# Kernel tuning notes

Measured on AMD Instinct MI355X. Metric: run time of the kernel, lower is better.

## Reference

```python
import jax, jax.numpy as jnp
import numpy as np

EPS = 1e-12  # F.normalize default eps


def _heatmap_pool(part_features, blocks):
    # part_features: [B, N, C]
    B, N, C = part_features.shape
    heatmap = jnp.mean(part_features, axis=-1)              # [B, N]
    arg = jnp.argsort(-heatmap, axis=1)                     # descending order
    x_sort = jnp.take_along_axis(part_features, arg[:, :, None], axis=1)  # [B, N, C]
    split_each = int(N / blocks)
    split_list = [split_each] * (blocks - 1)
    split_list.append(N - sum(split_list))
    offs = np.concatenate([[0], np.cumsum(split_list)])
    means = [jnp.mean(x_sort[:, offs[i]:offs[i + 1], :], axis=1) for i in range(blocks)]
    return jnp.stack(means, axis=2)                         # [B, C, blocks]


def _l2norm(x):
    n = jnp.sqrt(jnp.sum(x * x, axis=-1, keepdims=True))
    return x / jnp.maximum(n, EPS)


def setup_inputs() -> dict:
    key = jax.random.key(0)
    k1, k2 = jax.random.split(key)
    B, C, H, W = 64, 768, 24, 24
    return {
        "image_features1": jax.random.normal(k1, (B, C, H, W), dtype=jnp.float32),
        "image_features2": jax.random.normal(k2, (B, C, H, W), dtype=jnp.float32),
        "logit_scale": jnp.ones((1,), dtype=jnp.float32),
        "weights": jnp.ones((1,), dtype=jnp.float32),
        "blocks": 3,
    }


def reference(image_features1, image_features2, logit_scale, weights, blocks):
    B, C = image_features1.shape[0], image_features1.shape[1]
    f1 = image_features1.reshape(B, C, -1).transpose(0, 2, 1)  # [B, N, C]
    f2 = image_features2.reshape(B, C, -1).transpose(0, 2, 1)
    h1 = _heatmap_pool(f1, blocks)                             # [B, C, blocks]
    h2 = _heatmap_pool(f2, blocks)
    # cat blocks along channel dim: [B, C*blocks]
    b1 = jnp.concatenate([h1[:, :, i] for i in range(blocks)], axis=-1)
    b2 = jnp.concatenate([h2[:, :, i] for i in range(blocks)], axis=-1)
    n1 = _l2norm(b1)
    n2 = _l2norm(b2)
    return jnp.mean((n1 - n2) ** 2)
```

## Files before the change

### kernel.cpp

```cpp
#include <hip/hip_runtime.h>

#define NB 64
#define NC 768
#define NN 576
#define NF4 144

#define HR 16
#define HCH 48
#define GR 16
#define GCH 48

#define OFF_HM   0ull
#define SZ_HM    (2ull*NB*HCH*NN*8ull)
#define OFF_GID  (OFF_HM + SZ_HM)
#define SZ_GID   (2ull*NB*NN)
#define OFF_GP   (OFF_GID + SZ_GID)
#define SZ_GP    (2ull*NB*NC*12ull*4ull)
#define OFF_PB   (OFF_GP + SZ_GP)

__global__ __launch_bounds__(192, 8) void k_heat(const float* __restrict__ f1,
                                                 const float* __restrict__ f2,
                                                 double* __restrict__ hm) {
    int bx    = blockIdx.x;
    int inpb  = bx / HCH;
    int chunk = bx - inpb * HCH;
    int b     = inpb & (NB - 1);
    int inp   = inpb >> 6;
    const float* f = (inp ? f2 : f1) + (size_t)b * NC * NN + (size_t)chunk * HR * NN;
    int t = threadIdx.x;
    double d0 = 0, d1 = 0, d2 = 0;
    #pragma unroll
    for (int r0 = 0; r0 < HR; r0 += 8) {
        float v[24];
        #pragma unroll
        for (int rr = 0; rr < 8; ++rr) {
            const float* row = f + (size_t)(r0 + rr) * NN + t;
            v[rr * 3 + 0] = row[0];
            v[rr * 3 + 1] = row[192];
            v[rr * 3 + 2] = row[384];
        }
        #pragma unroll
        for (int rr = 0; rr < 8; ++rr) {
            d0 += (double)v[rr * 3 + 0];
            d1 += (double)v[rr * 3 + 1];
            d2 += (double)v[rr * 3 + 2];
        }
    }
    double* o = hm + (size_t)bx * NN;
    o[t] = d0; o[t + 192] = d1; o[t + 384] = d2;
}

__global__ __launch_bounds__(576) void k_rank(const double* __restrict__ hm,
                                              unsigned char* __restrict__ gid8) {
    int bx = blockIdx.x;
    int t  = threadIdx.x;
    const double* p = hm + (size_t)bx * HCH * NN + t;
    double h = 0;
    #pragma unroll
    for (int c0 = 0; c0 < HCH; c0 += 16) {
        double v[16];
        #pragma unroll
        for (int ch = 0; ch < 16; ++ch) v[ch] = p[(size_t)(c0 + ch) * NN];
        #pragma unroll
        for (int ch = 0; ch < 16; ++ch) h += v[ch];
    }
    __shared__ double hs[NN];
    hs[t] = h;
    __syncthreads();
    int cnt = 0;
    for (int j = 0; j < NN; ++j) {
        double hj = hs[j];
        cnt += (hj > h) ? 1 : ((hj == h && j < t) ? 1 : 0);
    }
    gid8[(size_t)bx * NN + t] = (cnt >= 384) ? 2 : ((cnt >= 192) ? 1 : 0);
}

__global__ __launch_bounds__(256, 8) void k_gsum(const float* __restrict__ f1,
                                                 const float* __restrict__ f2,
                                                 const unsigned* __restrict__ gidw,
                                                 float* __restrict__ gp) {
    int bx    = blockIdx.x;
    int inpb  = bx / GCH;
    int chunk = bx - inpb * GCH;
    int b     = inpb & (NB - 1);
    int inp   = inpb >> 6;
    const float4* plane = (const float4*)((inp ? f2 : f1) + (size_t)b * NC * NN);
    int t = threadIdx.x;
    int w = t >> 6, l = t & 63;
    int sub = l & 15, rr = l >> 4;

    unsigned g[9];
    const unsigned* gw = gidw + (size_t)inpb * NF4;
    #pragma unroll
    for (int k = 0; k < 9; ++k) g[k] = gw[sub + 16 * k];

    int c = chunk * GR + w * 4 + rr;
    const float4* row = plane + (size_t)c * NF4 + sub;
    float4 v[9];
    #pragma unroll
    for (int k = 0; k < 9; ++k) v[k] = row[16 * k];
    float sa = 0.f, s1 = 0.f, s2 = 0.f;
    #pragma unroll
    for (int k = 0; k < 9; ++k) {
        unsigned gwk = g[k];
        float x; unsigned gg;
        x = v[k].x; gg = gwk & 0xffu;         sa += x; s1 += (gg >= 1u) ? x : 0.f; s2 += (gg == 2u) ? x : 0.f;
        x = v[k].y; gg = (gwk >> 8) & 0xffu;  sa += x; s1 += (gg >= 1u) ? x : 0.f; s2 += (gg == 2u) ? x : 0.f;
        x = v[k].z; gg = (gwk >> 16) & 0xffu; sa += x; s1 += (gg >= 1u) ? x : 0.f; s2 += (gg == 2u) ? x : 0.f;
        x = v[k].w; gg = gwk >> 24;           sa += x; s1 += (gg >= 1u) ? x : 0.f; s2 += (gg == 2u) ? x : 0.f;
    }
    sa += __shfl_xor(sa, 4); s1 += __shfl_xor(s1, 4); s2 += __shfl_xor(s2, 4);
    sa += __shfl_xor(sa, 8); s1 += __shfl_xor(s1, 8); s2 += __shfl_xor(s2, 8);
    if (sub < 4) {
        float* o = gp + (size_t)inpb * NC * 12 + (size_t)c * 12;
        o[0 * 4 + sub] = sa - s1;
        o[1 * 4 + sub] = s1 - s2;
        o[2 * 4 + sub] = s2;
    }
}

__global__ __launch_bounds__(256) void k_mse(const float* __restrict__ gp,
                                             double* __restrict__ pb) {
    int b = blockIdx.x;
    int t = threadIdx.x;
    int w = t >> 6, l = t & 63;
    const float4* s1 = (const float4*)(gp + (size_t)b * NC * 12);
    const float4* s2 = (const float4*)(gp + (size_t)(NB + b) * NC * 12);

    double v1[9], v2[9];
    double q1 = 0, q2 = 0;
    #pragma unroll
    for (int k = 0; k < 9; ++k) {
        int e = t + 256 * k;
        float4 a = s1[e], c4 = s2[e];
        v1[k] = ((double)a.x + (double)a.y + (double)a.z + (double)a.w) * (1.0 / 192.0);
        v2[k] = ((double)c4.x + (double)c4.y + (double)c4.z + (double)c4.w) * (1.0 / 192.0);
        q1 += v1[k] * v1[k];
        q2 += v2[k] * v2[k];
    }
    #pragma unroll
    for (int m = 32; m; m >>= 1) { q1 += __shfl_xor(q1, m); q2 += __shfl_xor(q2, m); }
    __shared__ double red1[4], red2[4];
    if (l == 0) { red1[w] = q1; red2[w] = q2; }
    __syncthreads();
    q1 = red1[0] + red1[1] + red1[2] + red1[3];
    q2 = red2[0] + red2[1] + red2[2] + red2[3];
    double inv1 = 1.0 / fmax(sqrt(q1), 1e-12);
    double inv2 = 1.0 / fmax(sqrt(q2), 1e-12);

    double acc = 0;
    #pragma unroll
    for (int k = 0; k < 9; ++k) {
        double d = v1[k] * inv1 - v2[k] * inv2;
        acc += d * d;
    }
    #pragma unroll
    for (int m = 32; m; m >>= 1) acc += __shfl_xor(acc, m);
    __syncthreads();
    if (l == 0) red1[w] = acc;
    __syncthreads();
    if (t == 0) pb[b] = red1[0] + red1[1] + red1[2] + red1[3];
}

__global__ __launch_bounds__(64) void k_final(const double* __restrict__ pb,
                                              float* __restrict__ out) {
    int l = threadIdx.x;
    double v = pb[l];
    #pragma unroll
    for (int m = 32; m; m >>= 1) v += __shfl_xor(v, m);
    if (l == 0) out[0] = (float)(v / ((double)NB * 3.0 * (double)NC));
}

extern "C" void kernel_launch(void* const* d_in, const int* in_sizes, int n_in,
                              void* d_out, int out_size, void* d_ws, size_t ws_size,
                              hipStream_t stream) {
    (void)in_sizes; (void)n_in; (void)out_size; (void)ws_size;
    const float* f1 = (const float*)d_in[0];
    const float* f2 = (const float*)d_in[1];
    float* out = (float*)d_out;
    char* ws = (char*)d_ws;

    double*        hm   = (double*)(ws + OFF_HM);
    unsigned char* gid8 = (unsigned char*)(ws + OFF_GID);
    float*         gp   = (float*)(ws + OFF_GP);
    double*        pb   = (double*)(ws + OFF_PB);

    k_heat <<<2 * NB * HCH, 192, 0, stream>>>(f1, f2, hm);
    k_rank <<<2 * NB,       576, 0, stream>>>(hm, gid8);
    k_gsum <<<2 * NB * GCH, 256, 0, stream>>>(f1, f2, (const unsigned*)gid8, gp);
    k_mse  <<<NB,           256, 0, stream>>>(gp, pb);
    k_final<<<1,            64,  0, stream>>>(pb, out);
}
```

Baseline: 307.8 us.

## Pipeline heatmap and group-sum passes across the two inputs in a mixed kernel

Handles the two feature tensors in a staggered order. The heatmap pass for input 1 runs in the same launch as the group-sum pass for input 2, with blocks interleaved 3:4, so their memory traffic overlaps and the small serial rank kernel is hidden between larger launches. Group-sum blocks shrink to 192 threads covering 12 channels each (64 chunks per image), and launch bounds drop to 4 blocks per CU for the mixed kernels. The cost is one extra rank launch and more launches overall.

```diff
diff --git a/kernel.cpp b/kernel.cpp
--- a/kernel.cpp
+++ b/kernel.cpp
@@ -7,8 +7,8 @@
 
 #define HR 16
 #define HCH 48
-#define GR 16
-#define GCH 48
+#define GR 12
+#define GCH 64
 
 #define OFF_HM   0ull
 #define SZ_HM    (2ull*NB*HCH*NN*8ull)
@@ -18,23 +18,17 @@
 #define SZ_GP    (2ull*NB*NC*12ull*4ull)
 #define OFF_PB   (OFF_GP + SZ_GP)
 
-__global__ __launch_bounds__(192, 8) void k_heat(const float* __restrict__ f1,
-                                                 const float* __restrict__ f2,
-                                                 double* __restrict__ hm) {
-    int bx    = blockIdx.x;
-    int inpb  = bx / HCH;
-    int chunk = bx - inpb * HCH;
-    int b     = inpb & (NB - 1);
-    int inp   = inpb >> 6;
-    const float* f = (inp ? f2 : f1) + (size_t)b * NC * NN + (size_t)chunk * HR * NN;
-    int t = threadIdx.x;
+__device__ __forceinline__ void heat_body(const float* __restrict__ f,
+                                          double* __restrict__ hm,
+                                          int b, int chunk, int t) {
+    const float* p = f + (size_t)b * NC * NN + (size_t)chunk * HR * NN;
     double d0 = 0, d1 = 0, d2 = 0;
     #pragma unroll
     for (int r0 = 0; r0 < HR; r0 += 8) {
         float v[24];
         #pragma unroll
         for (int rr = 0; rr < 8; ++rr) {
-            const float* row = f + (size_t)(r0 + rr) * NN + t;
+            const float* row = p + (size_t)(r0 + rr) * NN + t;
             v[rr * 3 + 0] = row[0];
             v[rr * 3 + 1] = row[192];
             v[rr * 3 + 2] = row[384];
@@ -46,53 +40,22 @@
             d2 += (double)v[rr * 3 + 2];
         }
     }
-    double* o = hm + (size_t)bx * NN;
+    double* o = hm + ((size_t)b * HCH + chunk) * NN;
     o[t] = d0; o[t + 192] = d1; o[t + 384] = d2;
 }
 
-__global__ __launch_bounds__(576) void k_rank(const double* __restrict__ hm,
-                                              unsigned char* __restrict__ gid8) {
-    int bx = blockIdx.x;
-    int t  = threadIdx.x;
-    const double* p = hm + (size_t)bx * HCH * NN + t;
-    double h = 0;
-    #pragma unroll
-    for (int c0 = 0; c0 < HCH; c0 += 16) {
-        double v[16];
-        #pragma unroll
-        for (int ch = 0; ch < 16; ++ch) v[ch] = p[(size_t)(c0 + ch) * NN];
-        #pragma unroll
-        for (int ch = 0; ch < 16; ++ch) h += v[ch];
-    }
-    __shared__ double hs[NN];
-    hs[t] = h;
-    __syncthreads();
-    int cnt = 0;
-    for (int j = 0; j < NN; ++j) {
-        double hj = hs[j];
-        cnt += (hj > h) ? 1 : ((hj == h && j < t) ? 1 : 0);
-    }
-    gid8[(size_t)bx * NN + t] = (cnt >= 384) ? 2 : ((cnt >= 192) ? 1 : 0);
-}
-
-__global__ __launch_bounds__(256, 8) void k_gsum(const float* __restrict__ f1,
-                                                 const float* __restrict__ f2,
-                                                 const unsigned* __restrict__ gidw,
-                                                 float* __restrict__ gp) {
-    int bx    = blockIdx.x;
-    int inpb  = bx / GCH;
-    int chunk = bx - inpb * GCH;
-    int b     = inpb & (NB - 1);
-    int inp   = inpb >> 6;
-    const float4* plane = (const float4*)((inp ? f2 : f1) + (size_t)b * NC * NN);
-    int t = threadIdx.x;
+__device__ __forceinline__ void gsum_body(const float* __restrict__ f,
+                                          const unsigned* __restrict__ gw,
+                                          float* __restrict__ gp,
+                                          int b, int chunk, int t) {
+    const float4* plane = (const float4*)(f + (size_t)b * NC * NN);
     int w = t >> 6, l = t & 63;
     int sub = l & 15, rr = l >> 4;
 
     unsigned g[9];
-    const unsigned* gw = gidw + (size_t)inpb * NF4;
-    #pragma unroll
-    for (int k = 0; k < 9; ++k) g[k] = gw[sub + 16 * k];
+    const unsigned* gwb = gw + (size_t)b * NF4;
+    #pragma unroll
+    for (int k = 0; k < 9; ++k) g[k] = gwb[sub + 16 * k];
 
     int c = chunk * GR + w * 4 + rr;
     const float4* row = plane + (size_t)c * NF4 + sub;
@@ -112,11 +75,66 @@
     sa += __shfl_xor(sa, 4); s1 += __shfl_xor(s1, 4); s2 += __shfl_xor(s2, 4);
     sa += __shfl_xor(sa, 8); s1 += __shfl_xor(s1, 8); s2 += __shfl_xor(s2, 8);
     if (sub < 4) {
-        float* o = gp + (size_t)inpb * NC * 12 + (size_t)c * 12;
+        float* o = gp + (size_t)b * NC * 12 + (size_t)c * 12;
         o[0 * 4 + sub] = sa - s1;
         o[1 * 4 + sub] = s1 - s2;
         o[2 * 4 + sub] = s2;
     }
+}
+
+__global__ __launch_bounds__(192, 8) void k_heat(const float* __restrict__ f,
+                                                 double* __restrict__ hm) {
+    int bx = blockIdx.x;
+    int b = bx / HCH, chunk = bx - b * HCH;
+    heat_body(f, hm, b, chunk, threadIdx.x);
+}
+
+__global__ __launch_bounds__(192, 4) void k_mix(const float* __restrict__ fB,
+                                                double* __restrict__ hmB,
+                                                const float* __restrict__ fA,
+                                                const unsigned* __restrict__ gwA,
+                                                float* __restrict__ gpA) {
+    int bx = blockIdx.x, t = threadIdx.x;
+    int grp = bx / 7, r = bx - grp * 7;
+    if (r < 4) {
+        int gb = grp * 4 + r;
+        gsum_body(fA, gwA, gpA, gb >> 6, gb & 63, t);
+    } else {
+        int hb = grp * 3 + (r - 4);
+        heat_body(fB, hmB, hb / HCH, hb % HCH, t);
+    }
+}
+
+__global__ __launch_bounds__(192, 4) void k_gsum(const float* __restrict__ f,
+                                                 const unsigned* __restrict__ gw,
+                                                 float* __restrict__ gp) {
+    int bx = blockIdx.x;
+    gsum_body(f, gw, gp, bx >> 6, bx & 63, threadIdx.x);
+}
+
+__global__ __launch_bounds__(576) void k_rank(const double* __restrict__ hm,
+                                              unsigned char* __restrict__ gid8) {
+    int b = blockIdx.x;
+    int t = threadIdx.x;
+    const double* p = hm + (size_t)b * HCH * NN + t;
+    double h = 0;
+    #pragma unroll
+    for (int c0 = 0; c0 < HCH; c0 += 16) {
+        double v[16];
+        #pragma unroll
+        for (int ch = 0; ch < 16; ++ch) v[ch] = p[(size_t)(c0 + ch) * NN];
+        #pragma unroll
+        for (int ch = 0; ch < 16; ++ch) h += v[ch];
+    }
+    __shared__ double hs[NN];
+    hs[t] = h;
+    __syncthreads();
+    int cnt = 0;
+    for (int j = 0; j < NN; ++j) {
+        double hj = hs[j];
+        cnt += (hj > h) ? 1 : ((hj == h && j < t) ? 1 : 0);
+    }
+    gid8[(size_t)b * NN + t] = (cnt >= 384) ? 2 : ((cnt >= 192) ? 1 : 0);
 }
 
 __global__ __launch_bounds__(256) void k_mse(const float* __restrict__ gp,
@@ -180,14 +198,19 @@
     float* out = (float*)d_out;
     char* ws = (char*)d_ws;
 
-    double*        hm   = (double*)(ws + OFF_HM);
-    unsigned char* gid8 = (unsigned char*)(ws + OFF_GID);
-    float*         gp   = (float*)(ws + OFF_GP);
+    double*        hm1  = (double*)(ws + OFF_HM);
+    double*        hm2  = hm1 + (size_t)NB * HCH * NN;
+    unsigned char* gid1 = (unsigned char*)(ws + OFF_GID);
+    unsigned char* gid2 = gid1 + (size_t)NB * NN;
+    float*         gp1  = (float*)(ws + OFF_GP);
+    float*         gp2  = gp1 + (size_t)NB * NC * 12;
     double*        pb   = (double*)(ws + OFF_PB);
 
-    k_heat <<<2 * NB * HCH, 192, 0, stream>>>(f1, f2, hm);
-    k_rank <<<2 * NB,       576, 0, stream>>>(hm, gid8);
-    k_gsum <<<2 * NB * GCH, 256, 0, stream>>>(f1, f2, (const unsigned*)gid8, gp);
-    k_mse  <<<NB,           256, 0, stream>>>(gp, pb);
-    k_final<<<1,            64,  0, stream>>>(pb, out);
-}
+    k_heat <<<NB * HCH, 192, 0, stream>>>(f2, hm2);
+    k_rank <<<NB,       576, 0, stream>>>(hm2, gid2);
+    k_mix  <<<7 * 1024, 192, 0, stream>>>(f1, hm1, f2, (const unsigned*)gid2, gp2);
+    k_rank <<<NB,       576, 0, stream>>>(hm1, gid1);
+    k_gsum <<<NB * GCH, 192, 0, stream>>>(f1, (const unsigned*)gid1, gp1);
+    k_mse  <<<NB,       256, 0, stream>>>(gp1, pb);
+    k_final<<<1,        64,  0, stream>>>(pb, out);
+}
```

Result: slower. 316.3 us (+2.7%).
